# Performance work log

Hardware: AMD Instinct MI355X
Metric: run time of the kernel (lower is better)

Reference implementation:

```python
import jax, jax.numpy as jnp
import numpy as np
from jax import lax

B, C_IN, H, W = 16, 64, 128, 128
KH, KW, C_OUT = 3, 3, 128


def setup_inputs() -> dict:
    key = jax.random.key(0)
    k1, k2, k3, k4, k5 = jax.random.split(key, 5)
    x = jax.random.normal(k1, (B, C_IN, H, W), jnp.float32)
    # xavier-uniform-ish weight, layout [kh*kw*C_in, C_out] with patch ordering (kh, kw, c)
    limit = np.sqrt(6.0 / (KH * KW * C_IN + C_OUT)).astype(np.float32)
    w = jax.random.uniform(k2, (KH * KW * C_IN, C_OUT), jnp.float32, -limit, limit)
    b = jax.random.uniform(k3, (C_OUT,), jnp.float32)
    q = jax.random.uniform(k4, (1,), jnp.float32)
    p = jax.random.uniform(k5, (1,), jnp.float32)
    return {"x": x, "w": w, "b": b, "q": q, "p": p}


def reference(x, w, b, q, p):
    # Fused implicit-GEMM form of SCS: patch dot products and patch norms are
    # both expressed as convolutions, avoiding the im2col blowup.
    qe = jnp.exp(q[0])
    pe = jnp.exp(p[0])
    # torch patch layout after unfold+moveaxis is (kh, kw, C); w rows follow it
    w_conv = w.reshape(KH, KW, C_IN, C_OUT)  # HWIO
    dn = lax.conv_dimension_numbers(x.shape, w_conv.shape, ('NCHW', 'HWIO', 'NCHW'))
    pad = [(1, 1), (1, 1)]  # pad_len = k-1 = 2, split lo//2, rest (same as torch code)
    # s . k  -> [B, C_out, H, W]
    s_dot_k = lax.conv_general_dilated(x, w_conv, (1, 1), pad, dimension_numbers=dn)
    # ||s||_2 per patch (over kh, kw, C) -> [B, 1, H, W]
    ones_k = jnp.ones((KH, KW, C_IN, 1), x.dtype)
    patch_sq = lax.conv_general_dilated(x * x, ones_k, (1, 1), pad, dimension_numbers=dn)
    norm_s_q = jnp.sqrt(patch_sq) + qe
    norm_k_q = jnp.linalg.norm(w) + qe  # Frobenius norm of the whole weight matrix
    sim = s_dot_k / (norm_s_q * norm_k_q)
    out = jnp.sign(s_dot_k) * jnp.abs(sim) ** pe + b[None, :, None, None]
    return out  # [B, C_out, H, W]
```

## Files before the change

kernel.cpp:

```cpp
#include <hip/hip_runtime.h>
#include <hip/hip_bf16.h>
#include <math.h>

#define B_N 16
#define C_IN 64
#define H_N 128
#define W_N 128
#define C_OUT 128
#define RS 8448

typedef __attribute__((ext_vector_type(8))) short short8v;
typedef __attribute__((ext_vector_type(4))) float float4v;

__device__ __forceinline__ unsigned short f2bf(float f) {
  union { float f; unsigned u; } c; c.f = f;
  unsigned u = c.u + 0x7fffu + ((c.u >> 16) & 1u);
  return (unsigned short)(u >> 16);
}

__global__ __launch_bounds__(256) void scs_prep_w(
    const float* __restrict__ w, unsigned short* __restrict__ wf,
    float* __restrict__ partial)
{
  __shared__ float red[256];
  const int t    = threadIdx.x;
  const int gid  = blockIdx.x * 256 + t;
  const int frag = gid >> 6;
  const int l    = gid & 63;
  const int kh   = frag / 48;
  const int rem  = frag % 48;
  const int s    = rem >> 3;
  const int nt   = rem & 7;
  const int kb   = kh * 192 + s * 32 + (l >> 4) * 8;
  const int n    = nt * 16 + (l & 15);
  short8v pk;
  float ss = 0.f;
#pragma unroll
  for (int j = 0; j < 8; ++j) {
    const float v = w[(size_t)(kb + j) * C_OUT + n];
    ss = fmaf(v, v, ss);
    pk[j] = (short)f2bf(v);
  }
  *reinterpret_cast<short8v*>(wf + (size_t)frag * 512 + l * 8) = pk;
  red[t] = ss;
  __syncthreads();
  for (int off = 128; off > 0; off >>= 1) {
    if (t < off) red[t] += red[t + off];
    __syncthreads();
  }
  if (t == 0) partial[blockIdx.x] = red[0];
}

__global__ __launch_bounds__(512, 4) void scs_main(
    const float* __restrict__ x, const unsigned short* __restrict__ wf,
    const float* __restrict__ bias, const float* __restrict__ q,
    const float* __restrict__ p, const float* __restrict__ partial,
    float* __restrict__ out)
{
  __shared__ alignas(16) char xT[6 * RS];
  __shared__ float psacc[8][6][66];
  __shared__ float pl[4][64];

  const int t   = threadIdx.x;
  const int l   = t & 63;
  const int wid = t >> 6;
  const int wm  = wid >> 2;
  const int wn  = wid & 3;
  const int lr  = l & 15;
  const int lg  = l >> 4;
  const int bid = blockIdx.x;
  const int swz = (bid & 7) * 128 + (bid >> 3);
  const int b   = swz >> 6;
  const int rem = swz & 63;
  const int hs  = (rem >> 1) << 2;
  const int w0  = (rem & 1) << 6;

  const int wl = t & 63, gg = t >> 6;
  {
    const int jr = wl + 1;
    const int xb = jr * 128 + ((gg * 16) ^ ((jr & 7) << 4));
#pragma unroll
    for (int r = 0; r < 6; ++r) {
      const int  inr   = hs - 1 + r;
      const bool valid = (unsigned)inr < 128u;
      float ss = 0.f;
      if (valid) {
        const float* src = x + (((size_t)b * C_IN + gg * 8) * H_N + inr) * W_N + w0 + wl;
        float xv[8];
#pragma unroll
        for (int j = 0; j < 8; ++j) xv[j] = src[(size_t)j * H_N * W_N];
#pragma unroll
        for (int j = 0; j < 8; ++j) ss = fmaf(xv[j], xv[j], ss);
        union { __hip_bfloat162 h2[4]; short8v v; } pk;
#pragma unroll
        for (int j = 0; j < 4; ++j)
          pk.h2[j] = __float22bfloat162_rn(make_float2(xv[2 * j], xv[2 * j + 1]));
        *reinterpret_cast<short8v*>(xT + r * RS + xb) = pk.v;
      } else {
        *reinterpret_cast<short8v*>(xT + r * RS + xb) = short8v{0,0,0,0,0,0,0,0};
      }
      psacc[gg][r][jr] = ss;
    }
  }
  if (t < 96) {
    const int re  = t >> 4;
    const int sub = t & 15;
    const int ee  = sub & 1;
    const int ge  = sub >> 1;
    const int jr  = ee ? 65 : 0;
    const int gw  = w0 - 1 + ee * 65;
    const int inr = hs - 1 + re;
    const bool valid = ((unsigned)inr < 128u) && ((unsigned)gw < 128u);
    const int xb = re * RS + jr * 128 + ((ge * 16) ^ ((jr & 7) << 4));
    float ss = 0.f;
    if (valid) {
      const float* src = x + (((size_t)b * C_IN + ge * 8) * H_N + inr) * W_N + gw;
      float xv[8];
#pragma unroll
      for (int j = 0; j < 8; ++j) xv[j] = src[(size_t)j * H_N * W_N];
#pragma unroll
      for (int j = 0; j < 8; ++j) ss = fmaf(xv[j], xv[j], ss);
      union { __hip_bfloat162 h2[4]; short8v v; } pk;
#pragma unroll
      for (int j = 0; j < 4; ++j)
        pk.h2[j] = __float22bfloat162_rn(make_float2(xv[2 * j], xv[2 * j + 1]));
      *reinterpret_cast<short8v*>(xT + xb) = pk.v;
    } else {
      *reinterpret_cast<short8v*>(xT + xb) = short8v{0,0,0,0,0,0,0,0};
    }
    psacc[ge][re][jr] = ss;
  }

  const float bv0 = bias[wn * 32 + lr];
  const float bv1 = bias[wn * 32 + 16 + lr];

  __syncthreads();

  float4v acc[4][2][2];
#pragma unroll
  for (int o = 0; o < 4; ++o)
#pragma unroll
    for (int ml = 0; ml < 2; ++ml)
#pragma unroll
      for (int nl = 0; nl < 2; ++nl) acc[o][ml][nl] = float4v{0.f, 0.f, 0.f, 0.f};

  const int jbase = wm * 32 + lr;
#pragma unroll
  for (int s = 0; s < 6; ++s) {
    const int kw    = s >> 1;
    const int cslot = (s & 1) * 4 + lg;
    const int jlow  = (lr + kw) & 7;
    const int base_f = (jbase + kw) * 128 + ((cslot * 16) ^ (jlow << 4));

    short8v bfr[3][2];
#pragma unroll
    for (int kh = 0; kh < 3; ++kh) {
      const int fi = (kh * 6 + s) * 8 + wn * 2;
      bfr[kh][0] = *reinterpret_cast<const short8v*>(wf + (size_t)(fi + 0) * 512 + l * 8);
      bfr[kh][1] = *reinterpret_cast<const short8v*>(wf + (size_t)(fi + 1) * 512 + l * 8);
    }
#pragma unroll
    for (int r = 0; r < 6; ++r) {
      short8v a[2];
#pragma unroll
      for (int ml = 0; ml < 2; ++ml)
        a[ml] = *reinterpret_cast<const short8v*>(xT + r * RS + base_f + ml * 2048);
#pragma unroll
      for (int kh = 0; kh < 3; ++kh) {
        const int o = r - kh;
        if (o >= 0 && o < 4) {
#pragma unroll
          for (int ml = 0; ml < 2; ++ml)
#pragma unroll
            for (int nl = 0; nl < 2; ++nl)
              acc[o][ml][nl] = __builtin_amdgcn_mfma_f32_16x16x32_bf16(
                  a[ml], bfr[kh][nl], acc[o][ml][nl], 0, 0, 0);
        }
      }
    }
  }

  float ssum = 0.f;
#pragma unroll
  for (int i = 0; i < 36; ++i) ssum += partial[i];
  const float nk = sqrtf(ssum);
  const float qe = __builtin_amdgcn_exp2f(q[0] * 1.4426950408889634f);
  const float pe = __builtin_amdgcn_exp2f(p[0] * 1.4426950408889634f);
  const float nlg_nkq = -__builtin_amdgcn_logf(nk + qe);

  if (t < 256) {
    const int o   = t >> 6;
    const int wl2 = t & 63;
    const int jc  = wl2 + 1;
    float P = 0.f;
#pragma unroll
    for (int rr = 0; rr < 3; ++rr)
#pragma unroll
      for (int cc = 0; cc < 8; ++cc)
        P += psacc[cc][o + rr][jc - 1] + psacc[cc][o + rr][jc] + psacc[cc][o + rr][jc + 1];
    pl[o][wl2] = pe * (nlg_nkq - __builtin_amdgcn_logf(sqrtf(P) + qe));
  }
  __syncthreads();

#pragma unroll
  for (int o = 0; o < 4; ++o) {
    const int oh = hs + o;
#pragma unroll
    for (int ml = 0; ml < 2; ++ml) {
      const int wloc = wm * 32 + ml * 16 + lg * 4;
      const float4v plv = *reinterpret_cast<const float4v*>(&pl[o][wloc]);
#pragma unroll
      for (int nl = 0; nl < 2; ++nl) {
        const int n  = wn * 32 + nl * 16 + lr;
        const float bv = nl ? bv1 : bv0;
        float4v ov;
#pragma unroll
        for (int r = 0; r < 4; ++r) {
          const float sv  = acc[o][ml][nl][r];
          const float lg2 = __builtin_amdgcn_logf(fabsf(sv));
          const float e   = __builtin_amdgcn_exp2f(fmaf(pe, lg2, plv[r]));
          ov[r] = copysignf(e, sv) + bv;
        }
        *reinterpret_cast<float4v*>(
            out + (((size_t)b * C_OUT + n) * H_N + oh) * W_N + w0 + wloc) = ov;
      }
    }
  }
}

extern "C" void kernel_launch(void* const* d_in, const int* in_sizes, int n_in,
                              void* d_out, int out_size, void* d_ws, size_t ws_size,
                              hipStream_t stream) {
  const float* x = (const float*)d_in[0];
  const float* w = (const float*)d_in[1];
  const float* b = (const float*)d_in[2];
  const float* q = (const float*)d_in[3];
  const float* p = (const float*)d_in[4];
  float* out = (float*)d_out;
  float* partial = (float*)d_ws;
  unsigned short* wf = (unsigned short*)((char*)d_ws + 256);

  scs_prep_w<<<36, 256, 0, stream>>>(w, wf, partial);
  scs_main<<<B_N * (H_N / 4) * 2, 512, 0, stream>>>(x, wf, b, q, p, partial, out);
}
```

Before: 62.35 us.

## Stream input rows through ring buffer, overlapping global loads with MFMA over row pairs

Each block now covers an 8-row strip instead of 4 rows. It keeps a 6-slot ring buffer of bf16 input rows in LDS and loads the next rows from global memory while the MFMA k-steps for the current pair of output rows run. Patch-norm partial sums are reduced once per row into a shared array instead of being recomputed per output row. This cuts the 3-row halo reloads and hides load latency behind compute. In exchange the grid shrinks to 512 blocks, occupancy is lowered to 2 blocks per CU, and more barriers run per block.

```diff
diff --git a/kernel.cpp b/kernel.cpp
--- a/kernel.cpp
+++ b/kernel.cpp
@@ -51,7 +51,14 @@
   if (t == 0) partial[blockIdx.x] = red[0];
 }
 
-__global__ __launch_bounds__(512, 4) void scs_main(
+#define LGKM_BARRIER()                                   \
+  do {                                                   \
+    asm volatile("s_waitcnt lgkmcnt(0)" ::: "memory");   \
+    __builtin_amdgcn_s_barrier();                        \
+    asm volatile("" ::: "memory");                       \
+  } while (0)
+
+__global__ __launch_bounds__(512, 2) void scs_main(
     const float* __restrict__ x, const unsigned short* __restrict__ wf,
     const float* __restrict__ bias, const float* __restrict__ q,
     const float* __restrict__ p, const float* __restrict__ partial,
@@ -59,7 +66,8 @@
 {
   __shared__ alignas(16) char xT[6 * RS];
   __shared__ float psacc[8][6][66];
-  __shared__ float pl[4][64];
+  __shared__ float Ss[6][66];
+  __shared__ float pl[2][64];
 
   const int t   = threadIdx.x;
   const int l   = t & 63;
@@ -69,117 +77,97 @@
   const int lr  = l & 15;
   const int lg  = l >> 4;
   const int bid = blockIdx.x;
-  const int swz = (bid & 7) * 128 + (bid >> 3);
-  const int b   = swz >> 6;
-  const int rem = swz & 63;
-  const int hs  = (rem >> 1) << 2;
-  const int w0  = (rem & 1) << 6;
-
-  const int wl = t & 63, gg = t >> 6;
-  {
-    const int jr = wl + 1;
-    const int xb = jr * 128 + ((gg * 16) ^ ((jr & 7) << 4));
-#pragma unroll
-    for (int r = 0; r < 6; ++r) {
-      const int  inr   = hs - 1 + r;
-      const bool valid = (unsigned)inr < 128u;
-      float ss = 0.f;
-      if (valid) {
-        const float* src = x + (((size_t)b * C_IN + gg * 8) * H_N + inr) * W_N + w0 + wl;
-        float xv[8];
-#pragma unroll
-        for (int j = 0; j < 8; ++j) xv[j] = src[(size_t)j * H_N * W_N];
-#pragma unroll
-        for (int j = 0; j < 8; ++j) ss = fmaf(xv[j], xv[j], ss);
-        union { __hip_bfloat162 h2[4]; short8v v; } pk;
-#pragma unroll
-        for (int j = 0; j < 4; ++j)
-          pk.h2[j] = __float22bfloat162_rn(make_float2(xv[2 * j], xv[2 * j + 1]));
-        *reinterpret_cast<short8v*>(xT + r * RS + xb) = pk.v;
-      } else {
-        *reinterpret_cast<short8v*>(xT + r * RS + xb) = short8v{0,0,0,0,0,0,0,0};
-      }
-      psacc[gg][r][jr] = ss;
-    }
-  }
-  if (t < 96) {
-    const int re  = t >> 4;
-    const int sub = t & 15;
-    const int ee  = sub & 1;
-    const int ge  = sub >> 1;
-    const int jr  = ee ? 65 : 0;
-    const int gw  = w0 - 1 + ee * 65;
-    const int inr = hs - 1 + re;
-    const bool valid = ((unsigned)inr < 128u) && ((unsigned)gw < 128u);
-    const int xb = re * RS + jr * 128 + ((ge * 16) ^ ((jr & 7) << 4));
-    float ss = 0.f;
-    if (valid) {
-      const float* src = x + (((size_t)b * C_IN + ge * 8) * H_N + inr) * W_N + gw;
-      float xv[8];
-#pragma unroll
-      for (int j = 0; j < 8; ++j) xv[j] = src[(size_t)j * H_N * W_N];
-#pragma unroll
-      for (int j = 0; j < 8; ++j) ss = fmaf(xv[j], xv[j], ss);
-      union { __hip_bfloat162 h2[4]; short8v v; } pk;
-#pragma unroll
-      for (int j = 0; j < 4; ++j)
-        pk.h2[j] = __float22bfloat162_rn(make_float2(xv[2 * j], xv[2 * j + 1]));
-      *reinterpret_cast<short8v*>(xT + xb) = pk.v;
-    } else {
-      *reinterpret_cast<short8v*>(xT + xb) = short8v{0,0,0,0,0,0,0,0};
-    }
-    psacc[ge][re][jr] = ss;
-  }
-
-  const float bv0 = bias[wn * 32 + lr];
-  const float bv1 = bias[wn * 32 + 16 + lr];
-
-  __syncthreads();
-
-  float4v acc[4][2][2];
-#pragma unroll
-  for (int o = 0; o < 4; ++o)
-#pragma unroll
-    for (int ml = 0; ml < 2; ++ml)
-#pragma unroll
-      for (int nl = 0; nl < 2; ++nl) acc[o][ml][nl] = float4v{0.f, 0.f, 0.f, 0.f};
-
-  const int jbase = wm * 32 + lr;
-#pragma unroll
-  for (int s = 0; s < 6; ++s) {
-    const int kw    = s >> 1;
-    const int cslot = (s & 1) * 4 + lg;
-    const int jlow  = (lr + kw) & 7;
-    const int base_f = (jbase + kw) * 128 + ((cslot * 16) ^ (jlow << 4));
-
-    short8v bfr[3][2];
-#pragma unroll
-    for (int kh = 0; kh < 3; ++kh) {
-      const int fi = (kh * 6 + s) * 8 + wn * 2;
-      bfr[kh][0] = *reinterpret_cast<const short8v*>(wf + (size_t)(fi + 0) * 512 + l * 8);
-      bfr[kh][1] = *reinterpret_cast<const short8v*>(wf + (size_t)(fi + 1) * 512 + l * 8);
-    }
-#pragma unroll
-    for (int r = 0; r < 6; ++r) {
-      short8v a[2];
-#pragma unroll
-      for (int ml = 0; ml < 2; ++ml)
-        a[ml] = *reinterpret_cast<const short8v*>(xT + r * RS + base_f + ml * 2048);
-#pragma unroll
-      for (int kh = 0; kh < 3; ++kh) {
-        const int o = r - kh;
-        if (o >= 0 && o < 4) {
-#pragma unroll
-          for (int ml = 0; ml < 2; ++ml)
-#pragma unroll
-            for (int nl = 0; nl < 2; ++nl)
-              acc[o][ml][nl] = __builtin_amdgcn_mfma_f32_16x16x32_bf16(
-                  a[ml], bfr[kh][nl], acc[o][ml][nl], 0, 0, 0);
-        }
-      }
-    }
-  }
-
+  const int swz = (bid & 7) * 64 + (bid >> 3);
+  const int b     = swz >> 5;
+  const int strip = (swz >> 1) & 15;
+  const int w0    = (swz & 1) << 6;
+  const int hs    = strip << 3;
+
+  const int wl   = t & 63, gg = t >> 6;
+  const int jr_m = wl + 1;
+  const int xb_m = jr_m * 128 + ((gg * 16) ^ ((jr_m & 7) << 4));
+  const int e_jr = (t & 1) ? 65 : 0;
+  const int e_gw = w0 - 1 + (t & 1) * 65;
+  const int e_ge = (t >> 1) & 7;
+  const int e_xb = e_jr * 128 + ((e_ge * 16) ^ ((e_jr & 7) << 4));
+
+  float xrow[8], xedge[8];
+
+#define LOADM(row_)                                                           \
+  {                                                                           \
+    if ((unsigned)(row_) < 128u) {                                            \
+      const float* s_ = x + (((size_t)b * C_IN + gg * 8) * H_N + (row_)) * W_N + w0 + wl; \
+      _Pragma("unroll") for (int j = 0; j < 8; ++j) xrow[j] = s_[(size_t)j * H_N * W_N]; \
+    } else {                                                                  \
+      _Pragma("unroll") for (int j = 0; j < 8; ++j) xrow[j] = 0.f;            \
+    }                                                                         \
+    if (t < 16) {                                                             \
+      if (((unsigned)(row_) < 128u) && ((unsigned)e_gw < 128u)) {             \
+        const float* s_ = x + (((size_t)b * C_IN + e_ge * 8) * H_N + (row_)) * W_N + e_gw; \
+        _Pragma("unroll") for (int j = 0; j < 8; ++j) xedge[j] = s_[(size_t)j * H_N * W_N]; \
+      } else {                                                                \
+        _Pragma("unroll") for (int j = 0; j < 8; ++j) xedge[j] = 0.f;         \
+      }                                                                       \
+    }                                                                         \
+  }
+
+#define COMMITM(row_)                                                         \
+  {                                                                           \
+    const int sl_ = ((row_) + 6) % 6;                                         \
+    float ss_ = 0.f;                                                          \
+    _Pragma("unroll") for (int j = 0; j < 8; ++j) ss_ = fmaf(xrow[j], xrow[j], ss_); \
+    union { __hip_bfloat162 h2[4]; short8v v; } pk_;                          \
+    _Pragma("unroll") for (int j = 0; j < 4; ++j)                             \
+      pk_.h2[j] = __float22bfloat162_rn(make_float2(xrow[2*j], xrow[2*j+1])); \
+    *reinterpret_cast<short8v*>(xT + sl_ * RS + xb_m) = pk_.v;                \
+    psacc[gg][sl_][jr_m] = ss_;                                               \
+    if (t < 16) {                                                             \
+      float se_ = 0.f;                                                        \
+      _Pragma("unroll") for (int j = 0; j < 8; ++j) se_ = fmaf(xedge[j], xedge[j], se_); \
+      union { __hip_bfloat162 h2[4]; short8v v; } pe_;                        \
+      _Pragma("unroll") for (int j = 0; j < 4; ++j)                           \
+        pe_.h2[j] = __float22bfloat162_rn(make_float2(xedge[2*j], xedge[2*j+1])); \
+      *reinterpret_cast<short8v*>(xT + sl_ * RS + e_xb) = pe_.v;              \
+      psacc[e_ge][sl_][e_jr] = se_;                                           \
+    }                                                                         \
+  }
+
+#define KSTEP(s_)                                                             \
+  {                                                                           \
+    const int kw_    = (s_) >> 1;                                             \
+    const int cslot_ = ((s_) & 1) * 4 + lg;                                   \
+    const int jlow_  = (lr + kw_) & 7;                                        \
+    const int base_  = (jbase + kw_) * 128 + ((cslot_ * 16) ^ (jlow_ << 4));  \
+    short8v bfr_[3][2];                                                       \
+    _Pragma("unroll") for (int kh = 0; kh < 3; ++kh) {                        \
+      const int fi = (kh * 6 + (s_)) * 8 + wn * 2;                            \
+      bfr_[kh][0] = *reinterpret_cast<const short8v*>(wf + (size_t)(fi + 0) * 512 + l * 8); \
+      bfr_[kh][1] = *reinterpret_cast<const short8v*>(wf + (size_t)(fi + 1) * 512 + l * 8); \
+    }                                                                         \
+    _Pragma("unroll") for (int r = 0; r < 4; ++r) {                           \
+      short8v a_[2];                                                          \
+      _Pragma("unroll") for (int ml = 0; ml < 2; ++ml)                        \
+        a_[ml] = *reinterpret_cast<const short8v*>(xT + soff[r] + base_ + ml * 2048); \
+      if (r < 3) {                                                            \
+        _Pragma("unroll") for (int ml = 0; ml < 2; ++ml)                      \
+          _Pragma("unroll") for (int nl = 0; nl < 2; ++nl)                    \
+            acc[0][ml][nl] = __builtin_amdgcn_mfma_f32_16x16x32_bf16(         \
+                a_[ml], bfr_[r][nl], acc[0][ml][nl], 0, 0, 0);                \
+      }                                                                       \
+      if (r >= 1) {                                                           \
+        _Pragma("unroll") for (int ml = 0; ml < 2; ++ml)                      \
+          _Pragma("unroll") for (int nl = 0; nl < 2; ++nl)                    \
+            acc[1][ml][nl] = __builtin_amdgcn_mfma_f32_16x16x32_bf16(         \
+                a_[ml], bfr_[r - 1][nl], acc[1][ml][nl], 0, 0, 0);            \
+      }                                                                       \
+    }                                                                         \
+  }
+
+#pragma unroll
+  for (int r = 0; r < 4; ++r) {
+    LOADM(hs - 1 + r);
+    COMMITM(hs - 1 + r);
+  }
   float ssum = 0.f;
 #pragma unroll
   for (int i = 0; i < 36; ++i) ssum += partial[i];
@@ -187,42 +175,95 @@
   const float qe = __builtin_amdgcn_exp2f(q[0] * 1.4426950408889634f);
   const float pe = __builtin_amdgcn_exp2f(p[0] * 1.4426950408889634f);
   const float nlg_nkq = -__builtin_amdgcn_logf(nk + qe);
-
-  if (t < 256) {
-    const int o   = t >> 6;
-    const int wl2 = t & 63;
-    const int jc  = wl2 + 1;
-    float P = 0.f;
-#pragma unroll
-    for (int rr = 0; rr < 3; ++rr)
-#pragma unroll
-      for (int cc = 0; cc < 8; ++cc)
-        P += psacc[cc][o + rr][jc - 1] + psacc[cc][o + rr][jc] + psacc[cc][o + rr][jc + 1];
-    pl[o][wl2] = pe * (nlg_nkq - __builtin_amdgcn_logf(sqrtf(P) + qe));
-  }
+  const float bv0 = bias[wn * 32 + lr];
+  const float bv1 = bias[wn * 32 + 16 + lr];
   __syncthreads();
-
-#pragma unroll
-  for (int o = 0; o < 4; ++o) {
-    const int oh = hs + o;
-#pragma unroll
-    for (int ml = 0; ml < 2; ++ml) {
-      const int wloc = wm * 32 + ml * 16 + lg * 4;
-      const float4v plv = *reinterpret_cast<const float4v*>(&pl[o][wloc]);
-#pragma unroll
-      for (int nl = 0; nl < 2; ++nl) {
-        const int n  = wn * 32 + nl * 16 + lr;
-        const float bv = nl ? bv1 : bv0;
-        float4v ov;
-#pragma unroll
-        for (int r = 0; r < 4; ++r) {
-          const float sv  = acc[o][ml][nl][r];
-          const float lg2 = __builtin_amdgcn_logf(fabsf(sv));
-          const float e   = __builtin_amdgcn_exp2f(fmaf(pe, lg2, plv[r]));
-          ov[r] = copysignf(e, sv) + bv;
+  if (t < 264) {
+    const int rr = t / 66, jr = t % 66;
+    const int sl = (hs - 1 + rr + 6) % 6;
+    float s_ = 0.f;
+#pragma unroll
+    for (int g2 = 0; g2 < 8; ++g2) s_ += psacc[g2][sl][jr];
+    Ss[sl][jr] = s_;
+  }
+  __syncthreads();
+
+  const int jbase = wm * 32 + lr;
+#pragma unroll 1
+  for (int hp = 0; hp < 4; ++hp) {
+    const int h0 = hs + 2 * hp;
+    const bool last = (hp == 3);
+
+    int soff[4];
+#pragma unroll
+    for (int r = 0; r < 4; ++r) soff[r] = ((h0 - 1 + r + 6) % 6) * RS;
+
+    float4v acc[2][2][2];
+#pragma unroll
+    for (int o = 0; o < 2; ++o)
+#pragma unroll
+      for (int ml = 0; ml < 2; ++ml)
+#pragma unroll
+        for (int nl = 0; nl < 2; ++nl) acc[o][ml][nl] = float4v{0.f, 0.f, 0.f, 0.f};
+
+    if (!last) LOADM(h0 + 3);
+    KSTEP(0)
+    KSTEP(1)
+    if (!last) { COMMITM(h0 + 3); LOADM(h0 + 4); }
+    KSTEP(2)
+    KSTEP(3)
+    if (!last) COMMITM(h0 + 4);
+    KSTEP(4)
+    KSTEP(5)
+
+    LGKM_BARRIER();
+
+    if (!last && t < 132) {
+      const int rp = (t >= 66) ? 1 : 0;
+      const int jr = t - 66 * rp;
+      const int sl = (h0 + 3 + rp + 6) % 6;
+      float s_ = 0.f;
+#pragma unroll
+      for (int g2 = 0; g2 < 8; ++g2) s_ += psacc[g2][sl][jr];
+      Ss[sl][jr] = s_;
+    }
+    if (t < 128) {
+      const int o   = t >> 6;
+      const int wl2 = t & 63;
+      const int jc  = wl2 + 1;
+      float P = 0.f;
+#pragma unroll
+      for (int rr = 0; rr < 3; ++rr) {
+        const float* Sr = Ss[(h0 - 1 + o + rr + 6) % 6];
+        P += Sr[jc - 1] + Sr[jc] + Sr[jc + 1];
+      }
+      pl[o][wl2] = pe * (nlg_nkq - __builtin_amdgcn_logf(sqrtf(P) + qe));
+    }
+
+    LGKM_BARRIER();
+
+#pragma unroll
+    for (int o = 0; o < 2; ++o) {
+      const int oh = h0 + o;
+#pragma unroll
+      for (int ml = 0; ml < 2; ++ml) {
+        const int wloc = wm * 32 + ml * 16 + lg * 4;
+        const float4v plv = *reinterpret_cast<const float4v*>(&pl[o][wloc]);
+#pragma unroll
+        for (int nl = 0; nl < 2; ++nl) {
+          const int n  = wn * 32 + nl * 16 + lr;
+          const float bv = nl ? bv1 : bv0;
+          float4v ov;
+#pragma unroll
+          for (int r = 0; r < 4; ++r) {
+            const float sv  = acc[o][ml][nl][r];
+            const float lg2 = __builtin_amdgcn_logf(fabsf(sv));
+            const float e   = __builtin_amdgcn_exp2f(fmaf(pe, lg2, plv[r]));
+            ov[r] = copysignf(e, sv) + bv;
+          }
+          *reinterpret_cast<float4v*>(
+              out + (((size_t)b * C_OUT + n) * H_N + oh) * W_N + w0 + wloc) = ov;
         }
-        *reinterpret_cast<float4v*>(
-            out + (((size_t)b * C_OUT + n) * H_N + oh) * W_N + w0 + wloc) = ov;
       }
     }
   }
@@ -241,5 +282,5 @@
   unsigned short* wf = (unsigned short*)((char*)d_ws + 256);
 
   scs_prep_w<<<36, 256, 0, stream>>>(w, wf, partial);
-  scs_main<<<B_N * (H_N / 4) * 2, 512, 0, stream>>>(x, wf, b, q, p, partial, out);
-}
+  scs_main<<<512, 512, 0, stream>>>(x, wf, b, q, p, partial, out);
+}
```

New measurement: 69.32 us. 11.2% more time.
